# Kernel optimization log

Hardware: AMD Instinct MI355X
Metric: run time of the kernel (lower is better)

The kernel has to match this reference:

```python
import jax, jax.numpy as jnp
import numpy as np

UNITS = 32
ATT_WIDTH = 64


def setup_inputs() -> dict:
    key = jax.random.key(0)
    ks = jax.random.split(key, 4)
    B, T, F = 4, 1024, 256
    x = jax.random.normal(ks[0], (B, T, F), dtype=jnp.float32)
    Wt = jax.random.normal(ks[1], (F, UNITS), dtype=jnp.float32) * (1.0 / np.sqrt(F))
    Wx = jax.random.normal(ks[2], (F, UNITS), dtype=jnp.float32) * (1.0 / np.sqrt(F))
    bh = jnp.zeros((UNITS,), dtype=jnp.float32)
    Wa = jax.random.normal(ks[3], (UNITS, 1), dtype=jnp.float32) * (1.0 / np.sqrt(UNITS))
    ba = jnp.zeros((1,), dtype=jnp.float32)
    return {"x": x, "Wt": Wt, "Wx": Wx, "bh": bh, "Wa": Wa, "ba": ba}


def reference(x, Wt, Wx, bh, Wa, ba):
    # Additive (Bahdanau-style) self-attention emission:
    # h[b,t,s,u] = tanh(x[b,t] @ Wt + x[b,s] @ Wx + bh)
    q = jnp.einsum('btf,fu->btu', x, Wt)[:, :, None, :]   # [B,T,1,U]
    k = jnp.einsum('bsf,fu->bsu', x, Wx)[:, None, :, :]   # [B,1,T,U]
    h = jnp.tanh(q + k + bh)                               # [B,T,T,U]
    e = jnp.einsum('btsu,uo->bts', h, Wa) + ba[0]          # [B,T,T]

    # Local attention window (symmetric, width=ATT_WIDTH)
    T = x.shape[1]
    idx = jnp.arange(T)
    lower = idx - ATT_WIDTH // 2                           # [T]
    band = (lower[:, None] <= idx[None, :]) & (idx[None, :] < lower[:, None] + ATT_WIDTH)
    e = e - 10000.0 * (1.0 - band.astype(e.dtype))

    a = jax.nn.softmax(e, axis=-1)                         # [B,T,T]
    v = jnp.einsum('bts,bsf->btf', a, x)                   # [B,T,F]
    return v
```

## Files before the change

### kernel.cpp

```cpp
#include <hip/hip_runtime.h>
#include <math.h>

#define BB 4
#define TT 1024
#define FF 256
#define UU 32
#define HALF_W 32
#define WMAX 64
#define RB 8

__device__ __forceinline__ float fast_tanh(float x) {
    float e = __expf(2.0f * x);
    return 1.0f - 2.0f / (e + 1.0f);
}

__global__ __launch_bounds__(256) void qk_kernel(
    const float* __restrict__ x, const float* __restrict__ Wt,
    const float* __restrict__ Wx, const float* __restrict__ bh,
    float* __restrict__ qbuf, float* __restrict__ kbuf) {
    int row0 = blockIdx.x * RB;
    int tid = threadIdx.x;
    __shared__ float xs[RB][FF + 4];
    {
        const float4* src = (const float4*)(x + (size_t)row0 * FF);
#pragma unroll
        for (int i = 0; i < 2; ++i) {
            int p = tid + i * 256;
            int r = p >> 6;
            int c = p & 63;
            *(float4*)&xs[r][c * 4] = src[p];
        }
    }
    __syncthreads();

    int r    = tid >> 5;
    int sub  = tid & 31;
    int half = sub >> 4;
    int fh   = (sub >> 2) & 3;
    int ug   = (sub & 3) * 8;
    const float* __restrict__ W = half ? Wx : Wt;
    const float* __restrict__ xr = xs[r];

    float acc[8] = {0.f, 0.f, 0.f, 0.f, 0.f, 0.f, 0.f, 0.f};
#pragma unroll 4
    for (int it = 0; it < 16; ++it) {
        int f = 4 * fh + 16 * it;
        float4 x4 = *(const float4*)&xr[f];
#pragma unroll
        for (int j = 0; j < 4; ++j) {
            const float4* wp = (const float4*)(W + (size_t)(f + j) * UU + ug);
            float4 w0 = wp[0];
            float4 w1 = wp[1];
            float xv = (j == 0) ? x4.x : (j == 1) ? x4.y : (j == 2) ? x4.z : x4.w;
            acc[0] = fmaf(xv, w0.x, acc[0]);
            acc[1] = fmaf(xv, w0.y, acc[1]);
            acc[2] = fmaf(xv, w0.z, acc[2]);
            acc[3] = fmaf(xv, w0.w, acc[3]);
            acc[4] = fmaf(xv, w1.x, acc[4]);
            acc[5] = fmaf(xv, w1.y, acc[5]);
            acc[6] = fmaf(xv, w1.z, acc[6]);
            acc[7] = fmaf(xv, w1.w, acc[7]);
        }
    }
#pragma unroll
    for (int i = 0; i < 8; ++i) {
        acc[i] += __shfl_xor(acc[i], 4);
        acc[i] += __shfl_xor(acc[i], 8);
    }
    if (fh == 0) {
        int row = row0 + r;
        if (half == 0) {
            float4 b0 = *(const float4*)&bh[ug];
            float4 b1 = *(const float4*)&bh[ug + 4];
            float4 o0 = {acc[0] + b0.x, acc[1] + b0.y, acc[2] + b0.z, acc[3] + b0.w};
            float4 o1 = {acc[4] + b1.x, acc[5] + b1.y, acc[6] + b1.z, acc[7] + b1.w};
            *(float4*)&qbuf[(size_t)row * UU + ug]     = o0;
            *(float4*)&qbuf[(size_t)row * UU + ug + 4] = o1;
        } else {
            float4 o0 = {acc[0], acc[1], acc[2], acc[3]};
            float4 o1 = {acc[4], acc[5], acc[6], acc[7]};
            *(float4*)&kbuf[(size_t)row * UU + ug]     = o0;
            *(float4*)&kbuf[(size_t)row * UU + ug + 4] = o1;
        }
    }
}

__global__ __launch_bounds__(256) void attn_kernel(
    const float* __restrict__ x, const float* __restrict__ qbuf,
    const float* __restrict__ kbuf, const float* __restrict__ Wa,
    const float* __restrict__ ba, float* __restrict__ out) {
    int row = blockIdx.x;
    int t = row & (TT - 1);
    int b = row >> 10;
    int tid = threadIdx.x;
    int s0 = max(0, t - HALF_W);
    int s1 = min(TT, t + HALF_W);
    int W_ = s1 - s0;

    __shared__ float q_sh[UU];
    __shared__ float wa_sh[UU];
    __shared__ float e_sh[WMAX];
    __shared__ float a_sh[WMAX];
    __shared__ float4 red[4][64];

    if (tid < UU) {
        q_sh[tid]  = qbuf[(size_t)row * UU + tid];
        wa_sh[tid] = Wa[tid];
    }
    __syncthreads();

    int sl = tid >> 2;
    int j  = tid & 3;
    float partial = 0.f;
    if (sl < W_) {
        const float4* krow = (const float4*)(kbuf + (size_t)(b * TT + s0 + sl) * UU + j * 8);
        float4 k0 = krow[0];
        float4 k1 = krow[1];
        int u = j * 8;
        partial  = fast_tanh(q_sh[u + 0] + k0.x) * wa_sh[u + 0];
        partial += fast_tanh(q_sh[u + 1] + k0.y) * wa_sh[u + 1];
        partial += fast_tanh(q_sh[u + 2] + k0.z) * wa_sh[u + 2];
        partial += fast_tanh(q_sh[u + 3] + k0.w) * wa_sh[u + 3];
        partial += fast_tanh(q_sh[u + 4] + k1.x) * wa_sh[u + 4];
        partial += fast_tanh(q_sh[u + 5] + k1.y) * wa_sh[u + 5];
        partial += fast_tanh(q_sh[u + 6] + k1.z) * wa_sh[u + 6];
        partial += fast_tanh(q_sh[u + 7] + k1.w) * wa_sh[u + 7];
    }
    partial += __shfl_xor(partial, 1);
    partial += __shfl_xor(partial, 2);
    if (j == 0) e_sh[sl] = (sl < W_) ? partial + ba[0] : -1e30f;
    __syncthreads();

    if (tid < 64) {
        float e = e_sh[tid];
        float m = e;
#pragma unroll
        for (int off = 1; off < 64; off <<= 1) m = fmaxf(m, __shfl_xor(m, off));
        float p = __expf(e - m);
        float sum = p;
#pragma unroll
        for (int off = 1; off < 64; off <<= 1) sum += __shfl_xor(sum, off);
        a_sh[tid] = p / sum;
    }
    __syncthreads();

    int f4 = tid & 63;
    int w  = tid >> 6;
    const float4* xb4 = (const float4*)(x + (size_t)b * TT * FF);
    float4 acc = {0.f, 0.f, 0.f, 0.f};
#pragma unroll
    for (int i = 0; i < 16; ++i) {
        int s = w * 16 + i;
        int srow = min(s0 + s, TT - 1);
        float a = a_sh[s];
        float4 xv = xb4[(size_t)srow * (FF / 4) + f4];
        acc.x = fmaf(a, xv.x, acc.x);
        acc.y = fmaf(a, xv.y, acc.y);
        acc.z = fmaf(a, xv.z, acc.z);
        acc.w = fmaf(a, xv.w, acc.w);
    }
    red[w][f4] = acc;
    __syncthreads();
    if (tid < 64) {
        float4 r0 = red[0][tid], r1 = red[1][tid], r2 = red[2][tid], r3 = red[3][tid];
        float4 o = {r0.x + r1.x + r2.x + r3.x,
                    r0.y + r1.y + r2.y + r3.y,
                    r0.z + r1.z + r2.z + r3.z,
                    r0.w + r1.w + r2.w + r3.w};
        ((float4*)(out + (size_t)row * FF))[tid] = o;
    }
}

__global__ __launch_bounds__(256) void fused_kernel(
    const float* __restrict__ x, const float* __restrict__ Wt,
    const float* __restrict__ Wx, const float* __restrict__ bh,
    const float* __restrict__ Wa, const float* __restrict__ ba,
    float* __restrict__ out) {
    int row = blockIdx.x;
    int t = row & (TT - 1);
    int b = row >> 10;
    int tid = threadIdx.x;
    int s0 = max(0, t - HALF_W);
    int s1 = min(TT, t + HALF_W);
    int W_ = s1 - s0;

    __shared__ float ks[WMAX * UU];
    __shared__ float q_sh[UU];
    __shared__ float wa_sh[UU];
    __shared__ float e_sh[WMAX];
    __shared__ float a_sh[WMAX];

    if (tid < UU) {
        const float* xr = x + (size_t)row * FF;
        float acc = 0.f;
        for (int f = 0; f < FF; ++f) acc = fmaf(xr[f], Wt[f * UU + tid], acc);
        q_sh[tid]  = acc + bh[tid];
        wa_sh[tid] = Wa[tid];
    }
    for (int p = tid; p < W_ * UU; p += 256) {
        int sl = p >> 5, u = p & 31;
        const float* xr = x + (size_t)(b * TT + s0 + sl) * FF;
        float acc = 0.f;
        for (int f = 0; f < FF; ++f) acc = fmaf(xr[f], Wx[f * UU + u], acc);
        ks[p] = acc;
    }
    __syncthreads();

    int sl = tid >> 2;
    int j  = tid & 3;
    float partial = 0.f;
    if (sl < W_) {
#pragma unroll
        for (int uu = 0; uu < 8; ++uu) {
            int u = j * 8 + uu;
            partial += fast_tanh(q_sh[u] + ks[sl * UU + u]) * wa_sh[u];
        }
    }
    partial += __shfl_xor(partial, 1);
    partial += __shfl_xor(partial, 2);
    if (j == 0) e_sh[sl] = (sl < W_) ? partial + ba[0] : -1e30f;
    __syncthreads();

    if (tid < 64) {
        float e = e_sh[tid];
        float m = e;
#pragma unroll
        for (int off = 1; off < 64; off <<= 1) m = fmaxf(m, __shfl_xor(m, off));
        float p = __expf(e - m);
        float sum = p;
#pragma unroll
        for (int off = 1; off < 64; off <<= 1) sum += __shfl_xor(sum, off);
        a_sh[tid] = p / sum;
    }
    __syncthreads();

    float acc = 0.f;
    const float* xb = x + (size_t)(b * TT + s0) * FF + tid;
    for (int k2 = 0; k2 < W_; ++k2)
        acc = fmaf(a_sh[k2], xb[(size_t)k2 * FF], acc);
    out[(size_t)row * FF + tid] = acc;
}

extern "C" void kernel_launch(void* const* d_in, const int* in_sizes, int n_in,
                              void* d_out, int out_size, void* d_ws, size_t ws_size,
                              hipStream_t stream) {
    const float* x  = (const float*)d_in[0];
    const float* Wt = (const float*)d_in[1];
    const float* Wx = (const float*)d_in[2];
    const float* bh = (const float*)d_in[3];
    const float* Wa = (const float*)d_in[4];
    const float* ba = (const float*)d_in[5];
    float* out = (float*)d_out;

    const size_t need = (size_t)2 * BB * TT * UU * sizeof(float);
    if (ws_size >= need) {
        float* qbuf = (float*)d_ws;
        float* kbuf = qbuf + (size_t)BB * TT * UU;
        qk_kernel<<<BB * TT / RB, 256, 0, stream>>>(x, Wt, Wx, bh, qbuf, kbuf);
        attn_kernel<<<BB * TT, 256, 0, stream>>>(x, qbuf, kbuf, Wa, ba, out);
    } else {
        fused_kernel<<<BB * TT, 256, 0, stream>>>(x, Wt, Wx, bh, Wa, ba, out);
    }
}
```

Measured before the change: 88.98 us.

## Tile attention over 16 query rows per block with shared K and x reuse

Replaces the one-row-per-block attention kernel with a kernel that handles 16 query rows per block. The union K window is staged in shared memory, and each wavefront computes scores and softmax for four rows with one lane per key. In the weighted sum over x, each x row load is reused across four query rows. This is meant to cut redundant global loads of K and x and reduce the launch count from 4096 blocks to 256. The cost is fewer blocks to spread across CUs, more shared memory per block, and per-lane serial 32-unit tanh loops.

```diff
diff --git a/kernel.cpp b/kernel.cpp
--- a/kernel.cpp
+++ b/kernel.cpp
@@ -8,6 +8,8 @@
 #define HALF_W 32
 #define WMAX 64
 #define RB 8
+#define TCH 16
+#define NS_MAX 80
 
 __device__ __forceinline__ float fast_tanh(float x) {
     float e = __expf(2.0f * x);
@@ -85,54 +87,60 @@
     }
 }
 
-__global__ __launch_bounds__(256) void attn_kernel(
+__global__ __launch_bounds__(256) void attn2_kernel(
     const float* __restrict__ x, const float* __restrict__ qbuf,
     const float* __restrict__ kbuf, const float* __restrict__ Wa,
     const float* __restrict__ ba, float* __restrict__ out) {
-    int row = blockIdx.x;
-    int t = row & (TT - 1);
-    int b = row >> 10;
-    int tid = threadIdx.x;
-    int s0 = max(0, t - HALF_W);
-    int s1 = min(TT, t + HALF_W);
-    int W_ = s1 - s0;
-
-    __shared__ float q_sh[UU];
+    int blk  = blockIdx.x;
+    int b    = blk >> 6;
+    int t0   = (blk & 63) * TCH;
+    int tid  = threadIdx.x;
+    int lane = tid & 63;
+    int w    = tid >> 6;
+
+    int bs0 = max(0, t0 - HALF_W);
+    int bs1 = min(TT, t0 + TCH - 1 + HALF_W);
+    int NS  = bs1 - bs0;
+
+    __shared__ float k_sh[NS_MAX][UU + 1];
+    __shared__ float q_sh[TCH][UU];
     __shared__ float wa_sh[UU];
-    __shared__ float e_sh[WMAX];
-    __shared__ float a_sh[WMAX];
-    __shared__ float4 red[4][64];
-
-    if (tid < UU) {
-        q_sh[tid]  = qbuf[(size_t)row * UU + tid];
-        wa_sh[tid] = Wa[tid];
-    }
-    __syncthreads();
-
-    int sl = tid >> 2;
-    int j  = tid & 3;
-    float partial = 0.f;
-    if (sl < W_) {
-        const float4* krow = (const float4*)(kbuf + (size_t)(b * TT + s0 + sl) * UU + j * 8);
-        float4 k0 = krow[0];
-        float4 k1 = krow[1];
-        int u = j * 8;
-        partial  = fast_tanh(q_sh[u + 0] + k0.x) * wa_sh[u + 0];
-        partial += fast_tanh(q_sh[u + 1] + k0.y) * wa_sh[u + 1];
-        partial += fast_tanh(q_sh[u + 2] + k0.z) * wa_sh[u + 2];
-        partial += fast_tanh(q_sh[u + 3] + k0.w) * wa_sh[u + 3];
-        partial += fast_tanh(q_sh[u + 4] + k1.x) * wa_sh[u + 4];
-        partial += fast_tanh(q_sh[u + 5] + k1.y) * wa_sh[u + 5];
-        partial += fast_tanh(q_sh[u + 6] + k1.z) * wa_sh[u + 6];
-        partial += fast_tanh(q_sh[u + 7] + k1.w) * wa_sh[u + 7];
-    }
-    partial += __shfl_xor(partial, 1);
-    partial += __shfl_xor(partial, 2);
-    if (j == 0) e_sh[sl] = (sl < W_) ? partial + ba[0] : -1e30f;
-    __syncthreads();
-
-    if (tid < 64) {
-        float e = e_sh[tid];
+    __shared__ float a_sh[TCH][NS_MAX];
+
+    for (int p = tid; p < NS * 8; p += 256) {
+        int r  = p >> 3;
+        int u4 = (p & 7) * 4;
+        float4 v = *(const float4*)&kbuf[(size_t)(b * TT + bs0 + r) * UU + u4];
+        k_sh[r][u4 + 0] = v.x;
+        k_sh[r][u4 + 1] = v.y;
+        k_sh[r][u4 + 2] = v.z;
+        k_sh[r][u4 + 3] = v.w;
+    }
+    if (tid < TCH * 8) {
+        int r  = tid >> 3;
+        int u4 = (tid & 7) * 4;
+        float4 v = *(const float4*)&qbuf[(size_t)(b * TT + t0 + r) * UU + u4];
+        *(float4*)&q_sh[r][u4] = v;
+    }
+    if (tid < UU) wa_sh[tid] = Wa[tid];
+    for (int p = tid; p < TCH * NS_MAX; p += 256) ((float*)a_sh)[p] = 0.f;
+    float ba0 = ba[0];
+    __syncthreads();
+
+#pragma unroll
+    for (int i = 0; i < 4; ++i) {
+        int tl = w + 4 * i;
+        int tg = t0 + tl;
+        int s  = tg - HALF_W + lane;
+        float e = -1e30f;
+        if (s >= 0 && s < TT) {
+            int kr = s - bs0;
+            float acc = 0.f;
+#pragma unroll
+            for (int u = 0; u < UU; ++u)
+                acc += fast_tanh(q_sh[tl][u] + k_sh[kr][u]) * wa_sh[u];
+            e = acc + ba0;
+        }
         float m = e;
 #pragma unroll
         for (int off = 1; off < 64; off <<= 1) m = fmaxf(m, __shfl_xor(m, off));
@@ -140,35 +148,47 @@
         float sum = p;
 #pragma unroll
         for (int off = 1; off < 64; off <<= 1) sum += __shfl_xor(sum, off);
-        a_sh[tid] = p / sum;
-    }
-    __syncthreads();
-
-    int f4 = tid & 63;
-    int w  = tid >> 6;
-    const float4* xb4 = (const float4*)(x + (size_t)b * TT * FF);
-    float4 acc = {0.f, 0.f, 0.f, 0.f};
-#pragma unroll
-    for (int i = 0; i < 16; ++i) {
-        int s = w * 16 + i;
-        int srow = min(s0 + s, TT - 1);
-        float a = a_sh[s];
-        float4 xv = xb4[(size_t)srow * (FF / 4) + f4];
-        acc.x = fmaf(a, xv.x, acc.x);
-        acc.y = fmaf(a, xv.y, acc.y);
-        acc.z = fmaf(a, xv.z, acc.z);
-        acc.w = fmaf(a, xv.w, acc.w);
-    }
-    red[w][f4] = acc;
-    __syncthreads();
-    if (tid < 64) {
-        float4 r0 = red[0][tid], r1 = red[1][tid], r2 = red[2][tid], r3 = red[3][tid];
-        float4 o = {r0.x + r1.x + r2.x + r3.x,
-                    r0.y + r1.y + r2.y + r3.y,
-                    r0.z + r1.z + r2.z + r3.z,
-                    r0.w + r1.w + r2.w + r3.w};
-        ((float4*)(out + (size_t)row * FF))[tid] = o;
-    }
+        if (s >= 0 && s < TT) a_sh[tl][s - bs0] = p / sum;
+    }
+    __syncthreads();
+
+    int tg0 = t0 + 4 * w;
+    int sw0 = max(0, tg0 - HALF_W);
+    int sw1 = min(TT, tg0 + 3 + HALF_W);
+    const float4* __restrict__ xb = (const float4*)(x + (size_t)b * TT * FF);
+    const float* __restrict__ ar0 = a_sh[4 * w + 0];
+    const float* __restrict__ ar1 = a_sh[4 * w + 1];
+    const float* __restrict__ ar2 = a_sh[4 * w + 2];
+    const float* __restrict__ ar3 = a_sh[4 * w + 3];
+    float4 acc0 = {0.f, 0.f, 0.f, 0.f};
+    float4 acc1 = acc0, acc2 = acc0, acc3 = acc0;
+#pragma unroll 4
+    for (int s = sw0; s < sw1; ++s) {
+        float4 xv = xb[(size_t)s * (FF / 4) + lane];
+        int so = s - bs0;
+        float av0 = ar0[so], av1 = ar1[so], av2 = ar2[so], av3 = ar3[so];
+        acc0.x = fmaf(av0, xv.x, acc0.x);
+        acc0.y = fmaf(av0, xv.y, acc0.y);
+        acc0.z = fmaf(av0, xv.z, acc0.z);
+        acc0.w = fmaf(av0, xv.w, acc0.w);
+        acc1.x = fmaf(av1, xv.x, acc1.x);
+        acc1.y = fmaf(av1, xv.y, acc1.y);
+        acc1.z = fmaf(av1, xv.z, acc1.z);
+        acc1.w = fmaf(av1, xv.w, acc1.w);
+        acc2.x = fmaf(av2, xv.x, acc2.x);
+        acc2.y = fmaf(av2, xv.y, acc2.y);
+        acc2.z = fmaf(av2, xv.z, acc2.z);
+        acc2.w = fmaf(av2, xv.w, acc2.w);
+        acc3.x = fmaf(av3, xv.x, acc3.x);
+        acc3.y = fmaf(av3, xv.y, acc3.y);
+        acc3.z = fmaf(av3, xv.z, acc3.z);
+        acc3.w = fmaf(av3, xv.w, acc3.w);
+    }
+    float4* ob = (float4*)(out + (size_t)(b * TT + tg0) * FF);
+    ob[0 * (FF / 4) + lane] = acc0;
+    ob[1 * (FF / 4) + lane] = acc1;
+    ob[2 * (FF / 4) + lane] = acc2;
+    ob[3 * (FF / 4) + lane] = acc3;
 }
 
 __global__ __launch_bounds__(256) void fused_kernel(
@@ -257,7 +277,7 @@
         float* qbuf = (float*)d_ws;
         float* kbuf = qbuf + (size_t)BB * TT * UU;
         qk_kernel<<<BB * TT / RB, 256, 0, stream>>>(x, Wt, Wx, bh, qbuf, kbuf);
-        attn_kernel<<<BB * TT, 256, 0, stream>>>(x, qbuf, kbuf, Wa, ba, out);
+        attn2_kernel<<<BB * (TT / TCH), 256, 0, stream>>>(x, qbuf, kbuf, Wa, ba, out);
     } else {
         fused_kernel<<<BB * TT, 256, 0, stream>>>(x, Wt, Wx, bh, Wa, ba, out);
     }
```

New measurement: 91.53 us. +2.9%, slower.
